# Optimization experiments

Hardware: AMD Instinct MI355X
Metric: run time of the kernel (lower is better)

## Reference

```python
import jax, jax.numpy as jnp
import numpy as np

EMBED = 1024

def setup_inputs() -> dict:
    key = jax.random.key(0)
    ks = jax.random.split(key, 10)
    s = 1.0 / np.sqrt(EMBED)
    inp = {
        "target": jax.random.normal(ks[0], (8, 2048, EMBED), dtype=jnp.float32),
        "source": jax.random.normal(ks[1], (8, 2048, EMBED), dtype=jnp.float32),
        "Wq": jax.random.uniform(ks[2], (EMBED, EMBED), jnp.float32, -s, s),
        "bq": jax.random.uniform(ks[3], (EMBED,), jnp.float32, -s, s),
        "Wk": jax.random.uniform(ks[4], (EMBED, EMBED), jnp.float32, -s, s),
        "bk": jax.random.uniform(ks[5], (EMBED,), jnp.float32, -s, s),
        "Wv": jax.random.uniform(ks[6], (EMBED, EMBED), jnp.float32, -s, s),
        "bv": jax.random.uniform(ks[7], (EMBED,), jnp.float32, -s, s),
        "Wo": jax.random.uniform(ks[8], (EMBED, EMBED), jnp.float32, -s, s),
        "bo": jax.random.uniform(ks[9], (EMBED,), jnp.float32, -s, s),
    }
    return inp

def reference(target, source, Wq, bq, Wk, bk, Wv, bv, Wo, bo):
    # Linear layers (torch Linear: x @ W.T + b)
    Q = jnp.einsum('btd,ed->bte', target, Wq) + bq   # [B, Tq, D]
    K = jnp.einsum('bsd,ed->bse', source, Wk) + bk   # [B, Tk, D]
    V = jnp.einsum('bsd,ed->bse', source, Wv) + bv   # [B, Tk, D]
    d_k = Q.shape[-1]
    scores = jnp.einsum('bte,bse->bts', Q, K) / jnp.sqrt(jnp.float32(d_k))  # [B, Tq, Tk]
    attn = jax.nn.softmax(scores, axis=-1)
    out = jnp.einsum('bts,bse->bte', attn, V)        # [B, Tq, D]
    return jnp.einsum('bte,oe->bto', out, Wo) + bo
```

## Files before the change

### kernel.cpp

```cpp
#include <hip/hip_runtime.h>
#include <stdint.h>

typedef unsigned short bf16_t;
typedef __attribute__((ext_vector_type(8))) short   short8;
typedef __attribute__((ext_vector_type(4))) float   floatx4;
typedef __attribute__((ext_vector_type(4))) unsigned int   uint4v;
typedef __attribute__((ext_vector_type(4))) unsigned short ushort4v;

#define GAS __attribute__((address_space(1)))
#define LAS __attribute__((address_space(3)))

__device__ __forceinline__ unsigned short f2bf(float f) {
  unsigned u = __float_as_uint(f);
  u += 0x7FFFu + ((u >> 16) & 1u);
  return (unsigned short)(u >> 16);
}

__device__ __forceinline__ void g2l16(const bf16_t* g, bf16_t* l) {
  __builtin_amdgcn_global_load_lds((const GAS uint32_t*)g, (LAS uint32_t*)l, 16, 0, 0);
}

__global__ __launch_bounds__(256) void conv_f32_bf16(const float* __restrict__ s,
                                                     bf16_t* __restrict__ d) {
  size_t i = ((size_t)blockIdx.x * 256 + threadIdx.x) * 4;
  float4 v = *(const float4*)(s + i);
  ushort4v o = { f2bf(v.x), f2bf(v.y), f2bf(v.z), f2bf(v.w) };
  *(ushort4v*)(d + i) = o;
}

__global__ __launch_bounds__(256) void conv_w(const float* __restrict__ w0, const float* __restrict__ w1,
                                              const float* __restrict__ w2, const float* __restrict__ w3,
                                              bf16_t* __restrict__ d) {
  const float* s = blockIdx.y == 0 ? w0 : blockIdx.y == 1 ? w1 : blockIdx.y == 2 ? w2 : w3;
  size_t i = ((size_t)blockIdx.x * 256 + threadIdx.x) * 4;
  float4 v = *(const float4*)(s + i);
  ushort4v o = { f2bf(v.x), f2bf(v.y), f2bf(v.z), f2bf(v.w) };
  *(ushort4v*)(d + (size_t)blockIdx.y * 1048576 + i) = o;
}

template <typename OutT>
__global__ __launch_bounds__(512, 2) void gemm256(
    const bf16_t* __restrict__ A, const bf16_t* __restrict__ B,
    const float* __restrict__ bias, OutT* __restrict__ C,
    int M, int N, int K, long aBat, long bBat, long cBat, float scale)
{
  const int tid  = threadIdx.x;
  const int lane = tid & 63;
  const int wv   = tid >> 6;

  int bx, by, bz;
  {
    const int gx = gridDim.x, gy = gridDim.y, gz = gridDim.z;
    const int nwg = gx * gy * gz;
    int flat = (blockIdx.z * gy + blockIdx.y) * gx + blockIdx.x;
    if ((nwg & 7) == 0) {
      const int q = nwg >> 3;
      flat = (flat & 7) * q + (flat >> 3);
    }
    bx = flat % gx;
    const int rem = flat / gx;
    by = rem % gy;
    bz = rem / gy;
  }
  const int bm = by * 256;
  const int bn = bx * 256;
  A += (size_t)bz * aBat;
  B += (size_t)bz * bBat;
  C += (size_t)bz * cBat;

  __shared__ bf16_t sm[65536];

  const int nt = K >> 6;

  const int wm = (wv >> 2) * 128;
  const int wn = (wv & 3) * 64;

  const int fr = lane & 15;
  const int kq = lane >> 4;
  const int chE = kq ^ ((fr >> 1) & 3);
  const unsigned fA = (unsigned)((wm + fr) * 32 + chE * 8);
  const unsigned fB = (unsigned)((wn + fr) * 32 + chE * 8);

  const unsigned c0    = (unsigned)((tid & 3) ^ ((tid >> 3) & 3));
  const unsigned soff  = (unsigned)((tid >> 2) * K + c0 * 8);
  const unsigned kx128 = (unsigned)(K << 7);
  const unsigned lOff  = (unsigned)(wv * 512 + lane * 8);

  const bf16_t* gA = A + (size_t)bm * K;
  const bf16_t* gB = B + (size_t)bn * K;

#define SMA(b, kh) (sm + (((b) << 1) | (kh)) * 8192)
#define SMB(b, kh) (sm + 32768 + (((b) << 1) | (kh)) * 8192)
#define STG(gbase, lbase)                                   \
  do {                                                      \
    g2l16((gbase) + soff,         (lbase) + lOff);          \
    g2l16((gbase) + soff + kx128, (lbase) + lOff + 4096);   \
  } while (0)

  floatx4 acc[8][4];
  floatx4 zero = {0.0f, 0.0f, 0.0f, 0.0f};
#pragma unroll
  for (int i = 0; i < 8; i++)
#pragma unroll
    for (int j = 0; j < 4; j++) acc[i][j] = zero;

  STG(gA,      SMA(0, 0));
  STG(gB,      SMB(0, 0));
  STG(gA + 32, SMA(0, 1));
  STG(gB + 32, SMB(0, 1));
  if (nt > 1) {
    STG(gA + 64, SMA(1, 0));
    STG(gB + 64, SMB(1, 0));
    asm volatile("s_waitcnt vmcnt(4)" ::: "memory");
  } else {
    asm volatile("s_waitcnt vmcnt(0)" ::: "memory");
  }
  asm volatile("s_barrier" ::: "memory");

  int cur = 0;
  for (int t = 0; t < nt; ++t) {
    const int kc = t << 6;
    short8 a_[4], b_[4];
    const bf16_t* Ac0 = SMA(cur, 0);
    const bf16_t* Ac1 = SMA(cur, 1);
    const bf16_t* Bc0 = SMB(cur, 0);
    const bf16_t* Bc1 = SMB(cur, 1);

#pragma unroll
    for (int i = 0; i < 4; i++) a_[i] = *(const short8*)(Ac0 + fA + i * 512);
#pragma unroll
    for (int i = 0; i < 4; i++) b_[i] = *(const short8*)(Bc0 + fB + i * 512);
    if (t + 1 < nt) STG(gA + kc + 96, SMA(cur ^ 1, 1));
    asm volatile("s_barrier" ::: "memory");
    __builtin_amdgcn_s_setprio(1);
#pragma unroll
    for (int mi = 0; mi < 4; mi++)
#pragma unroll
      for (int ni = 0; ni < 4; ni++)
        acc[mi][ni] = __builtin_amdgcn_mfma_f32_16x16x32_bf16(a_[mi], b_[ni], acc[mi][ni], 0, 0, 0);
    __builtin_amdgcn_s_setprio(0);
    asm volatile("s_barrier" ::: "memory");

#pragma unroll
    for (int i = 0; i < 4; i++) a_[i] = *(const short8*)(Ac0 + fA + (4 + i) * 512);
    if (t + 1 < nt) STG(gB + kc + 96, SMB(cur ^ 1, 1));
    asm volatile("s_barrier" ::: "memory");
    __builtin_amdgcn_s_setprio(1);
#pragma unroll
    for (int mi = 0; mi < 4; mi++)
#pragma unroll
      for (int ni = 0; ni < 4; ni++)
        acc[4 + mi][ni] = __builtin_amdgcn_mfma_f32_16x16x32_bf16(a_[mi], b_[ni], acc[4 + mi][ni], 0, 0, 0);
    __builtin_amdgcn_s_setprio(0);
    asm volatile("s_barrier" ::: "memory");

#pragma unroll
    for (int i = 0; i < 4; i++) a_[i] = *(const short8*)(Ac1 + fA + i * 512);
#pragma unroll
    for (int i = 0; i < 4; i++) b_[i] = *(const short8*)(Bc1 + fB + i * 512);
    if (t + 2 < nt) STG(gA + kc + 128, SMA(cur, 0));
    asm volatile("s_barrier" ::: "memory");
    __builtin_amdgcn_s_setprio(1);
#pragma unroll
    for (int mi = 0; mi < 4; mi++)
#pragma unroll
      for (int ni = 0; ni < 4; ni++)
        acc[mi][ni] = __builtin_amdgcn_mfma_f32_16x16x32_bf16(a_[mi], b_[ni], acc[mi][ni], 0, 0, 0);
    __builtin_amdgcn_s_setprio(0);
    asm volatile("s_barrier" ::: "memory");

#pragma unroll
    for (int i = 0; i < 4; i++) a_[i] = *(const short8*)(Ac1 + fA + (4 + i) * 512);
    if (t + 2 < nt) STG(gB + kc + 128, SMB(cur, 0));
    asm volatile("s_barrier" ::: "memory");
    __builtin_amdgcn_s_setprio(1);
#pragma unroll
    for (int mi = 0; mi < 4; mi++)
#pragma unroll
      for (int ni = 0; ni < 4; ni++)
        acc[4 + mi][ni] = __builtin_amdgcn_mfma_f32_16x16x32_bf16(a_[mi], b_[ni], acc[4 + mi][ni], 0, 0, 0);
    __builtin_amdgcn_s_setprio(0);
    if (t + 2 < nt) asm volatile("s_waitcnt vmcnt(4)" ::: "memory");
    else            asm volatile("s_waitcnt vmcnt(0)" ::: "memory");
    asm volatile("s_barrier" ::: "memory");

    cur ^= 1;
  }
#undef STG
#undef SMB
#undef SMA

  __syncthreads();
  {
    const int er = (lane >> 4) * 4;
    const int ec = lane & 15;
    char* wreg = (char*)sm + wv * 16384;
#pragma unroll
    for (int pass = 0; pass < 2; ++pass) {
#pragma unroll
      for (int nf = 0; nf < 4; nf++) {
        const int lcol = nf * 16 + ec;
        const float bval = bias ? bias[bn + wn + lcol] : 0.0f;
#pragma unroll
        for (int mh = 0; mh < 4; mh++) {
#pragma unroll
          for (int r = 0; r < 4; r++) {
            float v = (acc[pass * 4 + mh][nf][r] + bval) * scale;
            const int row = mh * 16 + er + r;
            if constexpr (sizeof(OutT) == 4) {
              ((float*)wreg)[row * 64 + lcol] = v;
            } else {
              ((bf16_t*)wreg)[row * 64 + lcol] = f2bf(v);
            }
          }
        }
      }
      const size_t rbase = (size_t)(bm + wm + pass * 64);
      if constexpr (sizeof(OutT) == 4) {
        const float* tf = (const float*)wreg;
        float* Cf = (float*)C;
#pragma unroll
        for (int i = 0; i < 16; i++) {
          const int rr = i * 4 + (lane >> 4);
          floatx4 v = *(const floatx4*)(tf + rr * 64 + (lane & 15) * 4);
          *(floatx4*)(Cf + (rbase + rr) * N + bn + wn + (lane & 15) * 4) = v;
        }
      } else {
        const bf16_t* tb = (const bf16_t*)wreg;
        bf16_t* Cb = (bf16_t*)C;
#pragma unroll
        for (int i = 0; i < 8; i++) {
          const int rr = i * 8 + (lane >> 3);
          short8 v = *(const short8*)(tb + rr * 64 + (lane & 7) * 8);
          *(short8*)(Cb + (rbase + rr) * N + bn + wn + (lane & 7) * 8) = v;
        }
      }
    }
  }
}

__global__ __launch_bounds__(256) void softmax_rows(bf16_t* __restrict__ S) {
  const int tid = threadIdx.x;
  bf16_t* row = S + (size_t)blockIdx.x * 2048;
  uint4v raw = *(const uint4v*)(row + tid * 8);
  float x[8];
#pragma unroll
  for (int j = 0; j < 4; j++) {
    unsigned w = raw[j];
    x[2 * j]     = __uint_as_float(w << 16);
    x[2 * j + 1] = __uint_as_float(w & 0xFFFF0000u);
  }
  float m = -1e30f;
#pragma unroll
  for (int j = 0; j < 8; j++) m = fmaxf(m, x[j]);
  for (int o = 32; o > 0; o >>= 1) m = fmaxf(m, __shfl_xor(m, o, 64));
  __shared__ float red[4];
  if ((tid & 63) == 0) red[tid >> 6] = m;
  __syncthreads();
  m = fmaxf(fmaxf(red[0], red[1]), fmaxf(red[2], red[3]));

  float e[8];
  float s = 0.0f;
#pragma unroll
  for (int j = 0; j < 8; j++) { e[j] = __expf(x[j] - m); s += e[j]; }
  for (int o = 32; o > 0; o >>= 1) s += __shfl_xor(s, o, 64);
  __syncthreads();
  if ((tid & 63) == 0) red[tid >> 6] = s;
  __syncthreads();
  s = red[0] + red[1] + red[2] + red[3];
  float inv = 1.0f / s;

  uint4v o4;
#pragma unroll
  for (int j = 0; j < 4; j++) {
    unsigned lo = f2bf(e[2 * j] * inv);
    unsigned hi = f2bf(e[2 * j + 1] * inv);
    o4[j] = lo | (hi << 16);
  }
  *(uint4v*)(row + tid * 8) = o4;
}

__global__ __launch_bounds__(256) void transpose64(const bf16_t* __restrict__ V,
                                                   bf16_t* __restrict__ Vt) {
  __shared__ bf16_t t[64][72];
  const int tid = threadIdx.x;
  const int e0 = blockIdx.x * 64;
  const int s0 = blockIdx.y * 64;
  const size_t bb = (size_t)blockIdx.z * (2048 * 1024);
  const int r = tid >> 2;
  const int c = (tid & 3) * 16;
  const bf16_t* src = V + bb + (size_t)(s0 + r) * 1024 + e0 + c;
  uint4v v0 = *(const uint4v*)src;
  uint4v v1 = *(const uint4v*)(src + 8);
  *(uint4v*)&t[r][c]     = v0;
  *(uint4v*)&t[r][c + 8] = v1;
  __syncthreads();
  __attribute__((aligned(16))) bf16_t vals[16];
#pragma unroll
  for (int j = 0; j < 16; j++) vals[j] = t[c + j][r];
  bf16_t* dst = Vt + bb + (size_t)(e0 + r) * 2048 + s0 + c;
  *(uint4v*)dst       = *(const uint4v*)vals;
  *(uint4v*)(dst + 8) = *(const uint4v*)(vals + 8);
}

extern "C" void kernel_launch(void* const* d_in, const int* in_sizes, int n_in,
                              void* d_out, int out_size, void* d_ws, size_t ws_size,
                              hipStream_t stream) {
  const float* target = (const float*)d_in[0];
  const float* source = (const float*)d_in[1];
  const float* Wq = (const float*)d_in[2];
  const float* bq = (const float*)d_in[3];
  const float* Wk = (const float*)d_in[4];
  const float* bk = (const float*)d_in[5];
  const float* Wv = (const float*)d_in[6];
  const float* bv = (const float*)d_in[7];
  const float* Wo = (const float*)d_in[8];
  const float* bo = (const float*)d_in[9];
  float* out = (float*)d_out;

  char* ws = (char*)d_ws;
  bf16_t* Qb  = (bf16_t*)(ws + 0);
  bf16_t* Kb  = (bf16_t*)(ws + 33554432);
  bf16_t* Vt  = (bf16_t*)(ws + 67108864);
  bf16_t* Wb  = (bf16_t*)(ws + 100663296);
  bf16_t* Tb  = (bf16_t*)(ws + 109051904);
  bf16_t* Sb  = Tb;
  bf16_t* Srb = (bf16_t*)(ws + 142606336);
  bf16_t* Vb  = (bf16_t*)(ws + 176160768);
  bf16_t* AO  = Vb;

  conv_f32_bf16<<<16384, 256, 0, stream>>>(target, Tb);
  conv_f32_bf16<<<16384, 256, 0, stream>>>(source, Srb);
  conv_w<<<dim3(1024, 4), 256, 0, stream>>>(Wq, Wk, Wv, Wo, Wb);

  gemm256<<<dim3(4, 64, 1), 512, 0, stream>>>(Tb,  Wb,           bq, Qb, 16384, 1024, 1024, 0L, 0L, 0L, 0.03125f);
  gemm256<<<dim3(4, 64, 1), 512, 0, stream>>>(Srb, Wb + 1048576, bk, Kb, 16384, 1024, 1024, 0L, 0L, 0L, 1.0f);
  gemm256<<<dim3(4, 64, 1), 512, 0, stream>>>(Srb, Wb + 2097152, bv, Vb, 16384, 1024, 1024, 0L, 0L, 0L, 1.0f);

  transpose64<<<dim3(16, 32, 8), 256, 0, stream>>>(Vb, Vt);

  gemm256<<<dim3(8, 8, 8), 512, 0, stream>>>(Qb, Kb, (const float*)nullptr, Sb,
      2048, 2048, 1024, (long)2048 * 1024, (long)2048 * 1024, (long)2048 * 2048, 1.0f);

  softmax_rows<<<16384, 256, 0, stream>>>(Sb);

  gemm256<<<dim3(4, 8, 8), 512, 0, stream>>>(Sb, Vt, (const float*)nullptr, AO,
      2048, 1024, 2048, (long)2048 * 2048, (long)1024 * 2048, (long)2048 * 1024, 1.0f);

  gemm256<<<dim3(4, 64, 1), 512, 0, stream>>>(AO, Wb + 3145728, bo, out,
      16384, 1024, 1024, 0L, 0L, 0L, 1.0f);
}
```

Before: 502.3 us.

## Simplify GEMM pipeline to whole-tile double buffering with one barrier per step

Replaces the staggered half-tile prefetch, which used fine-grained vmcnt waits, per-phase s_barriers and setprio, with a plain double-buffered scheme. The next full K tile is issued at the top of each iteration and a single __syncthreads closes it. This removes many intra-iteration barriers and priority toggles and uses sched_barrier to keep the phases in order. In exchange, __syncthreads waits for all outstanding loads at the end of every iteration, so load latency overlaps only with the current tile's compute.

```diff
diff --git a/kernel.cpp b/kernel.cpp
--- a/kernel.cpp
+++ b/kernel.cpp
@@ -108,89 +108,69 @@
   STG(gB,      SMB(0, 0));
   STG(gA + 32, SMA(0, 1));
   STG(gB + 32, SMB(0, 1));
-  if (nt > 1) {
-    STG(gA + 64, SMA(1, 0));
-    STG(gB + 64, SMB(1, 0));
-    asm volatile("s_waitcnt vmcnt(4)" ::: "memory");
-  } else {
-    asm volatile("s_waitcnt vmcnt(0)" ::: "memory");
-  }
-  asm volatile("s_barrier" ::: "memory");
+  __syncthreads();
 
   int cur = 0;
   for (int t = 0; t < nt; ++t) {
     const int kc = t << 6;
-    short8 a_[4], b_[4];
+    if (t + 1 < nt) {
+      STG(gA + kc + 64, SMA(cur ^ 1, 0));
+      STG(gB + kc + 64, SMB(cur ^ 1, 0));
+      STG(gA + kc + 96, SMA(cur ^ 1, 1));
+      STG(gB + kc + 96, SMB(cur ^ 1, 1));
+    }
     const bf16_t* Ac0 = SMA(cur, 0);
     const bf16_t* Ac1 = SMA(cur, 1);
     const bf16_t* Bc0 = SMB(cur, 0);
     const bf16_t* Bc1 = SMB(cur, 1);
+    short8 a_[4], b_[4];
 
 #pragma unroll
     for (int i = 0; i < 4; i++) a_[i] = *(const short8*)(Ac0 + fA + i * 512);
 #pragma unroll
     for (int i = 0; i < 4; i++) b_[i] = *(const short8*)(Bc0 + fB + i * 512);
-    if (t + 1 < nt) STG(gA + kc + 96, SMA(cur ^ 1, 1));
-    asm volatile("s_barrier" ::: "memory");
-    __builtin_amdgcn_s_setprio(1);
 #pragma unroll
     for (int mi = 0; mi < 4; mi++)
 #pragma unroll
       for (int ni = 0; ni < 4; ni++)
         acc[mi][ni] = __builtin_amdgcn_mfma_f32_16x16x32_bf16(a_[mi], b_[ni], acc[mi][ni], 0, 0, 0);
-    __builtin_amdgcn_s_setprio(0);
-    asm volatile("s_barrier" ::: "memory");
+    __builtin_amdgcn_sched_barrier(0);
 
 #pragma unroll
     for (int i = 0; i < 4; i++) a_[i] = *(const short8*)(Ac0 + fA + (4 + i) * 512);
-    if (t + 1 < nt) STG(gB + kc + 96, SMB(cur ^ 1, 1));
-    asm volatile("s_barrier" ::: "memory");
-    __builtin_amdgcn_s_setprio(1);
 #pragma unroll
     for (int mi = 0; mi < 4; mi++)
 #pragma unroll
       for (int ni = 0; ni < 4; ni++)
         acc[4 + mi][ni] = __builtin_amdgcn_mfma_f32_16x16x32_bf16(a_[mi], b_[ni], acc[4 + mi][ni], 0, 0, 0);
-    __builtin_amdgcn_s_setprio(0);
-    asm volatile("s_barrier" ::: "memory");
+    __builtin_amdgcn_sched_barrier(0);
 
 #pragma unroll
     for (int i = 0; i < 4; i++) a_[i] = *(const short8*)(Ac1 + fA + i * 512);
 #pragma unroll
     for (int i = 0; i < 4; i++) b_[i] = *(const short8*)(Bc1 + fB + i * 512);
-    if (t + 2 < nt) STG(gA + kc + 128, SMA(cur, 0));
-    asm volatile("s_barrier" ::: "memory");
-    __builtin_amdgcn_s_setprio(1);
 #pragma unroll
     for (int mi = 0; mi < 4; mi++)
 #pragma unroll
       for (int ni = 0; ni < 4; ni++)
         acc[mi][ni] = __builtin_amdgcn_mfma_f32_16x16x32_bf16(a_[mi], b_[ni], acc[mi][ni], 0, 0, 0);
-    __builtin_amdgcn_s_setprio(0);
-    asm volatile("s_barrier" ::: "memory");
+    __builtin_amdgcn_sched_barrier(0);
 
 #pragma unroll
     for (int i = 0; i < 4; i++) a_[i] = *(const short8*)(Ac1 + fA + (4 + i) * 512);
-    if (t + 2 < nt) STG(gB + kc + 128, SMB(cur, 0));
-    asm volatile("s_barrier" ::: "memory");
-    __builtin_amdgcn_s_setprio(1);
 #pragma unroll
     for (int mi = 0; mi < 4; mi++)
 #pragma unroll
       for (int ni = 0; ni < 4; ni++)
         acc[4 + mi][ni] = __builtin_amdgcn_mfma_f32_16x16x32_bf16(a_[mi], b_[ni], acc[4 + mi][ni], 0, 0, 0);
-    __builtin_amdgcn_s_setprio(0);
-    if (t + 2 < nt) asm volatile("s_waitcnt vmcnt(4)" ::: "memory");
-    else            asm volatile("s_waitcnt vmcnt(0)" ::: "memory");
-    asm volatile("s_barrier" ::: "memory");
-
+
+    __syncthreads();
     cur ^= 1;
   }
 #undef STG
 #undef SMB
 #undef SMA
 
-  __syncthreads();
   {
     const int er = (lane >> 4) * 4;
     const int ec = lane & 15;
```

After: 509.3 us. Within noise of the previous version (+1.4%).
